# Kernel optimization log

Measured on AMD Instinct MI355X. Metric: run time of the kernel, lower is better.

The kernel has to match this reference:

```python
import jax, jax.numpy as jnp
import numpy as np

N = 1024    # num_points
HID = 1024  # Hamiltonian MLP hidden width


def setup_inputs() -> dict:
    key = jax.random.key(0)
    ks = jax.random.split(key, 6)
    def w(k, shape, fan_in):
        return jax.random.normal(k, shape, dtype=jnp.float32) / np.float32(np.sqrt(fan_in))
    return {
        "x": jax.random.normal(ks[0], (N,), dtype=jnp.float32),
        "q": jax.random.normal(ks[1], (N,), dtype=jnp.float32),
        "p": jax.random.normal(ks[2], (N,), dtype=jnp.float32),
        "W1": w(ks[3], (3 * N, HID), 3 * N),
        "b1": jnp.zeros((HID,), dtype=jnp.float32),
        "W2": w(ks[4], (HID, HID), HID),
        "b2": jnp.zeros((HID,), dtype=jnp.float32),
        "W3": w(ks[5], (HID, 1), HID),
        "b3": jnp.zeros((1,), dtype=jnp.float32),
    }


def _hamiltonian(z, W1, b1, W2, b2, W3, b3):
    # H: R^{3N} -> scalar (matches self.H(cat([x,q,p])).sum())
    h = jnp.tanh(z @ W1 + b1)
    h = jnp.tanh(h @ W2 + b2)
    return jnp.sum(h @ W3 + b3)


def reference(x, q, p, W1, b1, W2, b2, W3, b3):
    n = x.shape[0]

    def grads_qp(x_):
        # (dH/dq, dH/dp) as a function of x, with q,p closed over
        f = lambda q_, p_: _hamiltonian(jnp.concatenate([x_, q_, p_]), W1, b1, W2, b2, W3, b3)
        return jax.grad(f, argnums=(0, 1))(q, p)  # each [n]

    # Diagonal of cross-Hessian blocks via forward-over-reverse, batched over
    # all n basis directions at once (replaces the per-index autograd loop).
    eye = jnp.eye(n, dtype=x.dtype)

    def diag_entry(e_i, i):
        _, (dgq, dgp) = jax.jvp(grads_qp, (x,), (e_i,))
        return dgq[i], dgp[i]  # d2H/(dx_i dq_i), d2H/(dx_i dp_i)

    dH_dq_dx, dH_dp_dx = jax.vmap(diag_entry)(eye, jnp.arange(n))  # each [n]
    return dH_dp_dx, -dH_dq_dx
```

## Files before the change

kernel.cpp:

```cpp
#include <hip/hip_runtime.h>
#include <math.h>

typedef unsigned short u16;
typedef __bf16 bf16x8 __attribute__((ext_vector_type(8)));
typedef float f32x4 __attribute__((ext_vector_type(4)));

__device__ inline u16 bf16_rn(float x) {
    unsigned u = __float_as_uint(x);
    return (u16)((u + 0x7FFFu + ((u >> 16) & 1u)) >> 16);
}
__device__ inline uint2 pack4(u16 a, u16 b, u16 c, u16 d) {
    uint2 r;
    r.x = (unsigned)a | ((unsigned)b << 16);
    r.y = (unsigned)c | ((unsigned)d << 16);
    return r;
}
__device__ inline uint2 pack4f(float a, float b, float c, float d) {
    return pack4(bf16_rn(a), bf16_rn(b), bf16_rn(c), bf16_rn(d));
}
__device__ inline f32x4 mfma16(bf16x8 a, bf16x8 b, f32x4 c) {
    return __builtin_amdgcn_mfma_f32_16x16x32_bf16(a, b, c, 0, 0, 0);
}

__global__ __launch_bounds__(256) void k_pre(const float* __restrict__ x,
                                             const float* __restrict__ q,
                                             const float* __restrict__ p,
                                             const float* __restrict__ W1,
                                             u16* __restrict__ Ah,
                                             float* __restrict__ Upart,
                                             float* __restrict__ out,
                                             float* __restrict__ Vacc) {
    int b = blockIdx.x, t = threadIdx.x;
    if (b < 1024) {
        int idx = (b * 256 + t) * 4;
        float4 v = *(const float4*)(W1 + idx);
        *(uint2*)&Ah[idx] = pack4f(v.x, v.y, v.z, v.w);
    } else if (b < 1216) {
        int jc = b - 1024;
        int k = (jc & 3) * 256 + t;
        int j0 = (jc >> 2) * 64;
        __shared__ float zs[64];
        if (t < 64) {
            int j = j0 + t;
            zs[t] = (j < 1024) ? x[j] : (j < 2048 ? q[j - 1024] : p[j - 2048]);
        }
        __syncthreads();
        float acc = 0.f;
#pragma unroll 8
        for (int j = 0; j < 64; ++j) acc += zs[j] * W1[(j0 + j) * 1024 + k];
        Upart[(jc >> 2) * 1024 + k] = acc;
    } else {
        int idx = ((b - 1216) * 256 + t) * 4;
        if (idx < 2048) *(float4*)(out + idx) = make_float4(0.f, 0.f, 0.f, 0.f);
        else *(float4*)(Vacc + idx - 2048) = make_float4(0.f, 0.f, 0.f, 0.f);
    }
}

__global__ __launch_bounds__(256) void k_w2v(const float* __restrict__ W2,
                                             const float* __restrict__ b1,
                                             const float* __restrict__ Upart,
                                             float* __restrict__ H1g, float* __restrict__ D1g,
                                             u16* __restrict__ W2h,
                                             u16* __restrict__ WTh,
                                             float* __restrict__ Vacc) {
    __shared__ float T[64][65];
    __shared__ float hs[64], ds[64];
    int k0 = blockIdx.y * 64, m0 = blockIdx.x * 64;
    int t = threadIdx.x;
    if (t < 64) {
        float u = 0.f;
#pragma unroll 8
        for (int c = 0; c < 48; ++c) u += Upart[c * 1024 + k0 + t];
        float h = tanhf(u + b1[k0 + t]);
        hs[t] = h;
        ds[t] = 1.f - h * h;
        if (m0 == 0) { H1g[k0 + t] = h; D1g[k0 + t] = 1.f - h * h; }
    }
    __syncthreads();
    int rr = t >> 4, cc = (t & 15) * 4;
    float4 vp = make_float4(0.f, 0.f, 0.f, 0.f);
#pragma unroll
    for (int j = 0; j < 4; ++j) {
        int r = rr + j * 16;
        float4 v = *(const float4*)(W2 + (k0 + r) * 1024 + m0 + cc);
        T[r][cc + 0] = v.x; T[r][cc + 1] = v.y; T[r][cc + 2] = v.z; T[r][cc + 3] = v.w;
        *(uint2*)&W2h[(k0 + r) * 1024 + m0 + cc] = pack4f(v.x, v.y, v.z, v.w);
        float hk = hs[r];
        vp.x += hk * v.x; vp.y += hk * v.y; vp.z += hk * v.z; vp.w += hk * v.w;
    }
    vp.x += __shfl_xor(vp.x, 16); vp.y += __shfl_xor(vp.y, 16);
    vp.z += __shfl_xor(vp.z, 16); vp.w += __shfl_xor(vp.w, 16);
    vp.x += __shfl_xor(vp.x, 32); vp.y += __shfl_xor(vp.y, 32);
    vp.z += __shfl_xor(vp.z, 32); vp.w += __shfl_xor(vp.w, 32);
    if (((t & 63) >> 4) == 0) {
        atomicAdd(&Vacc[m0 + cc + 0], vp.x);
        atomicAdd(&Vacc[m0 + cc + 1], vp.y);
        atomicAdd(&Vacc[m0 + cc + 2], vp.z);
        atomicAdd(&Vacc[m0 + cc + 3], vp.w);
    }
    __syncthreads();
#pragma unroll
    for (int j = 0; j < 4; ++j) {
        int mrow = rr + j * 16;
        float f0 = T[cc + 0][mrow] * ds[cc + 0];
        float f1 = T[cc + 1][mrow] * ds[cc + 1];
        float f2 = T[cc + 2][mrow] * ds[cc + 2];
        float f3 = T[cc + 3][mrow] * ds[cc + 3];
        *(uint2*)&WTh[(m0 + mrow) * 1024 + k0 + cc] = pack4f(f0, f1, f2, f3);
    }
}

#define LDK 68
__global__ __launch_bounds__(512) void k_gemm1(const u16* __restrict__ Ah,
                                               const u16* __restrict__ Bh,
                                               const float* __restrict__ Vacc,
                                               const float* __restrict__ b2,
                                               const float* __restrict__ W3,
                                               const float* __restrict__ W2,
                                               const float* __restrict__ H1,
                                               const float* __restrict__ D1,
                                               float* __restrict__ Avec,
                                               u16* __restrict__ Sh) {
    __shared__ u16 As[2][64 * LDK];
    __shared__ u16 Bs[2][64 * LDK];
    __shared__ float sv[1024];
    int tid = threadIdx.x;
    if (blockIdx.x == 16) {
        int kbase = blockIdx.y * 64;
#pragma unroll
        for (int j = 0; j < 2; ++j) {
            int m = tid + j * 512;
            float h = tanhf(Vacc[m] + b2[m]);
            sv[m] = (1.f - h * h) * W3[m];
        }
        __syncthreads();
        int g = tid >> 3, sub = tid & 7;
        int k = kbase + g;
        const float* wrow = W2 + k * 1024 + sub * 128;
        const float* svp = sv + sub * 128;
        float acc = 0.f;
#pragma unroll 8
        for (int j = 0; j < 128; ++j) acc += wrow[j] * svp[j];
        acc += __shfl_xor(acc, 1);
        acc += __shfl_xor(acc, 2);
        acc += __shfl_xor(acc, 4);
        if (sub == 0) Avec[k] = -2.f * H1[k] * D1[k] * acc;
        return;
    }
    int lane = tid & 63, wv = tid >> 6;
    int kh = wv >> 2, wy = (wv >> 1) & 1, wx = wv & 1;
    int i0 = blockIdx.y * 64, m0 = blockIdx.x * 64;
    int srow = tid >> 3, sseg = (tid & 7) * 8;
    int ldso = srow * LDK + sseg;
    const u16* ap = Ah + (i0 + srow) * 1024 + sseg;
    const u16* bp = Bh + (m0 + srow) * 1024 + sseg;
    int tx = lane & 15, qy = lane >> 4;
    int koff = kh * 32 + qy * 8;
    int raA[2], rbB[2];
    raA[0] = (wy * 32 + tx) * LDK + koff;
    raA[1] = raA[0] + 16 * LDK;
    rbB[0] = (wx * 32 + tx) * LDK + koff;
    rbB[1] = rbB[0] + 16 * LDK;
    f32x4 acc[2][2];
#pragma unroll
    for (int a = 0; a < 2; ++a)
#pragma unroll
        for (int b = 0; b < 2; ++b) acc[a][b] = (f32x4){0.f, 0.f, 0.f, 0.f};

    *(uint4*)&As[0][ldso] = *(const uint4*)(ap);
    *(uint4*)&Bs[0][ldso] = *(const uint4*)(bp);

    for (int k0 = 0; k0 < 1024; k0 += 64) {
        int buf = (k0 >> 6) & 1;
        int kn = (k0 + 64) & 1023;
        uint4 pa = *(const uint4*)(ap + kn);
        uint4 pc = *(const uint4*)(bp + kn);
        __syncthreads();
        bf16x8 aH0 = *(const bf16x8*)&As[buf][raA[0]];
        bf16x8 aH1 = *(const bf16x8*)&As[buf][raA[1]];
        bf16x8 bH0 = *(const bf16x8*)&Bs[buf][rbB[0]];
        bf16x8 bH1 = *(const bf16x8*)&Bs[buf][rbB[1]];
        acc[0][0] = mfma16(aH0, bH0, acc[0][0]);
        acc[0][1] = mfma16(aH0, bH1, acc[0][1]);
        acc[1][0] = mfma16(aH1, bH0, acc[1][0]);
        acc[1][1] = mfma16(aH1, bH1, acc[1][1]);
        int nb = buf ^ 1;
        *(uint4*)&As[nb][ldso] = pa;
        *(uint4*)&Bs[nb][ldso] = pc;
    }
    __syncthreads();
    f32x4* mrg = (f32x4*)&As[0][0];
    if (kh == 1) {
#pragma unroll
        for (int si = 0; si < 2; ++si)
#pragma unroll
            for (int sj = 0; sj < 2; ++sj)
                mrg[(((wy * 2 + wx) * 4 + si * 2 + sj) * 4 + qy) * 16 + tx] = acc[si][sj];
    }
    __syncthreads();
    if (kh == 0) {
#pragma unroll
        for (int si = 0; si < 2; ++si)
#pragma unroll
            for (int sj = 0; sj < 2; ++sj) {
                f32x4 o = mrg[(((wy * 2 + wx) * 4 + si * 2 + sj) * 4 + qy) * 16 + tx];
                acc[si][sj][0] += o[0]; acc[si][sj][1] += o[1];
                acc[si][sj][2] += o[2]; acc[si][sj][3] += o[3];
            }
#pragma unroll
        for (int sj = 0; sj < 2; ++sj) {
            int m = m0 + wx * 32 + sj * 16 + tx;
            float hv = tanhf(Vacc[m] + b2[m]);
            float d2 = 1.f - hv * hv;
            float cm = -2.f * hv * d2 * W3[m];
#pragma unroll
            for (int si = 0; si < 2; ++si) {
                int ib = i0 + wy * 32 + si * 16 + qy * 4;
#pragma unroll
                for (int r = 0; r < 4; ++r)
                    Sh[(ib + r) * 1024 + m] = bf16_rn(acc[si][sj][r] * cm);
            }
        }
    }
}

__global__ __launch_bounds__(512) void k_gemm2(const u16* __restrict__ Sh,
                                               const u16* __restrict__ W2h,
                                               const float* __restrict__ W1,
                                               const float* __restrict__ D1,
                                               const float* __restrict__ Avec,
                                               float* __restrict__ out) {
    __shared__ u16 As[2][64 * LDK];
    __shared__ u16 Bs[2][64 * LDK];
    int tid = threadIdx.x, lane = tid & 63, wv = tid >> 6;
    int kh = wv >> 2, wy = (wv >> 1) & 1, wx = wv & 1;
    int i0 = blockIdx.y * 64, k0g = blockIdx.x * 64;
    int srow = tid >> 3, sseg = (tid & 7) * 8;
    int ldso = srow * LDK + sseg;
    const u16* ap = Sh + (i0 + srow) * 1024 + sseg;
    const u16* bp = W2h + (k0g + srow) * 1024 + sseg;
    int tx = lane & 15, qy = lane >> 4;
    int koff = kh * 32 + qy * 8;
    int raA[2], rbB[2];
    raA[0] = (wy * 32 + tx) * LDK + koff;
    raA[1] = raA[0] + 16 * LDK;
    rbB[0] = (wx * 32 + tx) * LDK + koff;
    rbB[1] = rbB[0] + 16 * LDK;
    f32x4 acc[2][2];
#pragma unroll
    for (int a = 0; a < 2; ++a)
#pragma unroll
        for (int b = 0; b < 2; ++b) acc[a][b] = (f32x4){0.f, 0.f, 0.f, 0.f};

    *(uint4*)&As[0][ldso] = *(const uint4*)(ap);
    *(uint4*)&Bs[0][ldso] = *(const uint4*)(bp);

    for (int m0 = 0; m0 < 1024; m0 += 64) {
        int buf = (m0 >> 6) & 1;
        int mn = (m0 + 64) & 1023;
        uint4 pa = *(const uint4*)(ap + mn);
        uint4 pc = *(const uint4*)(bp + mn);
        __syncthreads();
        bf16x8 aH0 = *(const bf16x8*)&As[buf][raA[0]];
        bf16x8 aH1 = *(const bf16x8*)&As[buf][raA[1]];
        bf16x8 bH0 = *(const bf16x8*)&Bs[buf][rbB[0]];
        bf16x8 bH1 = *(const bf16x8*)&Bs[buf][rbB[1]];
        acc[0][0] = mfma16(aH0, bH0, acc[0][0]);
        acc[0][1] = mfma16(aH0, bH1, acc[0][1]);
        acc[1][0] = mfma16(aH1, bH0, acc[1][0]);
        acc[1][1] = mfma16(aH1, bH1, acc[1][1]);
        int nb = buf ^ 1;
        *(uint4*)&As[nb][ldso] = pa;
        *(uint4*)&Bs[nb][ldso] = pc;
    }
    __syncthreads();
    f32x4* mrg = (f32x4*)&As[0][0];
    if (kh == 1) {
#pragma unroll
        for (int si = 0; si < 2; ++si)
#pragma unroll
            for (int sj = 0; sj < 2; ++sj)
                mrg[(((wy * 2 + wx) * 4 + si * 2 + sj) * 4 + qy) * 16 + tx] = acc[si][sj];
    }
    __syncthreads();
    if (kh == 0) {
#pragma unroll
        for (int si = 0; si < 2; ++si)
#pragma unroll
            for (int sj = 0; sj < 2; ++sj) {
                f32x4 o = mrg[(((wy * 2 + wx) * 4 + si * 2 + sj) * 4 + qy) * 16 + tx];
                acc[si][sj][0] += o[0]; acc[si][sj][1] += o[1];
                acc[si][sj][2] += o[2]; acc[si][sj][3] += o[3];
            }
        int kk[2];
        float d1v[2], avv[2];
#pragma unroll
        for (int sj = 0; sj < 2; ++sj) {
            kk[sj] = k0g + wx * 32 + sj * 16 + tx;
            d1v[sj] = D1[kk[sj]];
            avv[sj] = Avec[kk[sj]];
        }
#pragma unroll
        for (int si = 0; si < 2; ++si) {
            int ib = i0 + wy * 32 + si * 16 + qy * 4;
#pragma unroll
            for (int r = 0; r < 4; ++r) {
                int i = ib + r;
                float pq = 0.f, pp = 0.f;
#pragma unroll
                for (int sj = 0; sj < 2; ++sj) {
                    int k = kk[sj];
                    float dr = avv[sj] * W1[i * 1024 + k] + d1v[sj] * acc[si][sj][r];
                    pq += W1[(1024 + i) * 1024 + k] * dr;
                    pp += W1[(2048 + i) * 1024 + k] * dr;
                }
                for (int o = 1; o < 16; o <<= 1) {
                    pq += __shfl_xor(pq, o);
                    pp += __shfl_xor(pp, o);
                }
                if (tx == 0) {
                    atomicAdd(&out[i], pp);
                    atomicAdd(&out[1024 + i], -pq);
                }
            }
        }
    }
}

extern "C" void kernel_launch(void* const* d_in, const int* in_sizes, int n_in,
                              void* d_out, int out_size, void* d_ws, size_t ws_size,
                              hipStream_t stream) {
    const float* x = (const float*)d_in[0];
    const float* q = (const float*)d_in[1];
    const float* p = (const float*)d_in[2];
    const float* W1 = (const float*)d_in[3];
    const float* b1 = (const float*)d_in[4];
    const float* W2 = (const float*)d_in[5];
    const float* b2 = (const float*)d_in[6];
    const float* W3 = (const float*)d_in[7];
    float* out = (float*)d_out;
    float* ws = (float*)d_ws;
    float* H1 = ws, *D1 = ws + 1024, *Avec = ws + 2048, *Vacc = ws + 3072;
    float* Upart = ws + 4096;
    u16* u0 = (u16*)(ws + 65536);
    u16* Ah = u0;
    u16* WTh = u0 + 1048576;
    u16* W2h = u0 + 2097152;
    u16* Sh = u0 + 3145728;

    k_pre<<<1219, 256, 0, stream>>>(x, q, p, W1, Ah, Upart, out, Vacc);
    k_w2v<<<dim3(16, 16), 256, 0, stream>>>(W2, b1, Upart, H1, D1, W2h, WTh, Vacc);
    k_gemm1<<<dim3(17, 16), 512, 0, stream>>>(Ah, WTh, Vacc, b2, W3, W2, H1, D1, Avec, Sh);
    k_gemm2<<<dim3(16, 16), 512, 0, stream>>>(Sh, W2h, W1, D1, Avec, out);
}
```

Measured before the change: 120.0 us.

## Fuse W1 bf16 conversion into matvec, parallelize Upart reduce, deepen GEMM prefetch

The first 1024 rows of W1 are now converted to bf16 inside the z·W1 partial matvec blocks that already read them, so the separate conversion blocks go away and W1 is read once instead of twice. k_w2v spreads the 48-way Upart reduction over all 256 threads in four groups instead of only 64 threads. Both GEMM kernels prefetch global tiles two iterations ahead instead of one, which uses more registers. The fused conversion loop stores scalar u16 values with less parallelism (192 blocks), which may limit bandwidth.

```diff
diff --git a/kernel.cpp b/kernel.cpp
--- a/kernel.cpp
+++ b/kernel.cpp
@@ -31,12 +31,8 @@
                                              float* __restrict__ out,
                                              float* __restrict__ Vacc) {
     int b = blockIdx.x, t = threadIdx.x;
-    if (b < 1024) {
-        int idx = (b * 256 + t) * 4;
-        float4 v = *(const float4*)(W1 + idx);
-        *(uint2*)&Ah[idx] = pack4f(v.x, v.y, v.z, v.w);
-    } else if (b < 1216) {
-        int jc = b - 1024;
+    if (b < 192) {
+        int jc = b;
         int k = (jc & 3) * 256 + t;
         int j0 = (jc >> 2) * 64;
         __shared__ float zs[64];
@@ -46,11 +42,20 @@
         }
         __syncthreads();
         float acc = 0.f;
+        if (j0 < 1024) {
 #pragma unroll 8
-        for (int j = 0; j < 64; ++j) acc += zs[j] * W1[(j0 + j) * 1024 + k];
+            for (int j = 0; j < 64; ++j) {
+                float v = W1[(j0 + j) * 1024 + k];
+                Ah[(j0 + j) * 1024 + k] = bf16_rn(v);
+                acc += zs[j] * v;
+            }
+        } else {
+#pragma unroll 8
+            for (int j = 0; j < 64; ++j) acc += zs[j] * W1[(j0 + j) * 1024 + k];
+        }
         Upart[(jc >> 2) * 1024 + k] = acc;
     } else {
-        int idx = ((b - 1216) * 256 + t) * 4;
+        int idx = ((b - 192) * 256 + t) * 4;
         if (idx < 2048) *(float4*)(out + idx) = make_float4(0.f, 0.f, 0.f, 0.f);
         else *(float4*)(Vacc + idx - 2048) = make_float4(0.f, 0.f, 0.f, 0.f);
     }
@@ -65,12 +70,19 @@
                                              float* __restrict__ Vacc) {
     __shared__ float T[64][65];
     __shared__ float hs[64], ds[64];
+    __shared__ float red[4][64];
     int k0 = blockIdx.y * 64, m0 = blockIdx.x * 64;
     int t = threadIdx.x;
+    {
+        int lk = t & 63, g = t >> 6;
+        float u = 0.f;
+#pragma unroll
+        for (int c = 0; c < 12; ++c) u += Upart[(g * 12 + c) * 1024 + k0 + lk];
+        red[g][lk] = u;
+    }
+    __syncthreads();
     if (t < 64) {
-        float u = 0.f;
-#pragma unroll 8
-        for (int c = 0; c < 48; ++c) u += Upart[c * 1024 + k0 + t];
+        float u = red[0][t] + red[1][t] + red[2][t] + red[3][t];
         float h = tanhf(u + b1[k0 + t]);
         hs[t] = h;
         ds[t] = 1.f - h * h;
@@ -167,14 +179,16 @@
 #pragma unroll
         for (int b = 0; b < 2; ++b) acc[a][b] = (f32x4){0.f, 0.f, 0.f, 0.f};
 
+    uint4 pa1 = *(const uint4*)(ap + 64);
+    uint4 pc1 = *(const uint4*)(bp + 64);
     *(uint4*)&As[0][ldso] = *(const uint4*)(ap);
     *(uint4*)&Bs[0][ldso] = *(const uint4*)(bp);
 
     for (int k0 = 0; k0 < 1024; k0 += 64) {
         int buf = (k0 >> 6) & 1;
-        int kn = (k0 + 64) & 1023;
-        uint4 pa = *(const uint4*)(ap + kn);
-        uint4 pc = *(const uint4*)(bp + kn);
+        int kn2 = (k0 + 128) & 1023;
+        uint4 pa2 = *(const uint4*)(ap + kn2);
+        uint4 pc2 = *(const uint4*)(bp + kn2);
         __syncthreads();
         bf16x8 aH0 = *(const bf16x8*)&As[buf][raA[0]];
         bf16x8 aH1 = *(const bf16x8*)&As[buf][raA[1]];
@@ -185,8 +199,9 @@
         acc[1][0] = mfma16(aH1, bH0, acc[1][0]);
         acc[1][1] = mfma16(aH1, bH1, acc[1][1]);
         int nb = buf ^ 1;
-        *(uint4*)&As[nb][ldso] = pa;
-        *(uint4*)&Bs[nb][ldso] = pc;
+        *(uint4*)&As[nb][ldso] = pa1;
+        *(uint4*)&Bs[nb][ldso] = pc1;
+        pa1 = pa2; pc1 = pc2;
     }
     __syncthreads();
     f32x4* mrg = (f32x4*)&As[0][0];
@@ -252,14 +267,16 @@
 #pragma unroll
         for (int b = 0; b < 2; ++b) acc[a][b] = (f32x4){0.f, 0.f, 0.f, 0.f};
 
+    uint4 pa1 = *(const uint4*)(ap + 64);
+    uint4 pc1 = *(const uint4*)(bp + 64);
     *(uint4*)&As[0][ldso] = *(const uint4*)(ap);
     *(uint4*)&Bs[0][ldso] = *(const uint4*)(bp);
 
     for (int m0 = 0; m0 < 1024; m0 += 64) {
         int buf = (m0 >> 6) & 1;
-        int mn = (m0 + 64) & 1023;
-        uint4 pa = *(const uint4*)(ap + mn);
-        uint4 pc = *(const uint4*)(bp + mn);
+        int mn2 = (m0 + 128) & 1023;
+        uint4 pa2 = *(const uint4*)(ap + mn2);
+        uint4 pc2 = *(const uint4*)(bp + mn2);
         __syncthreads();
         bf16x8 aH0 = *(const bf16x8*)&As[buf][raA[0]];
         bf16x8 aH1 = *(const bf16x8*)&As[buf][raA[1]];
@@ -270,8 +287,9 @@
         acc[1][0] = mfma16(aH1, bH0, acc[1][0]);
         acc[1][1] = mfma16(aH1, bH1, acc[1][1]);
         int nb = buf ^ 1;
-        *(uint4*)&As[nb][ldso] = pa;
-        *(uint4*)&Bs[nb][ldso] = pc;
+        *(uint4*)&As[nb][ldso] = pa1;
+        *(uint4*)&Bs[nb][ldso] = pc1;
+        pa1 = pa2; pc1 = pc2;
     }
     __syncthreads();
     f32x4* mrg = (f32x4*)&As[0][0];
@@ -348,7 +366,7 @@
     u16* W2h = u0 + 2097152;
     u16* Sh = u0 + 3145728;
 
-    k_pre<<<1219, 256, 0, stream>>>(x, q, p, W1, Ah, Upart, out, Vacc);
+    k_pre<<<195, 256, 0, stream>>>(x, q, p, W1, Ah, Upart, out, Vacc);
     k_w2v<<<dim3(16, 16), 256, 0, stream>>>(W2, b1, Upart, H1, D1, W2h, WTh, Vacc);
     k_gemm1<<<dim3(17, 16), 512, 0, stream>>>(Ah, WTh, Vacc, b2, W3, W2, H1, D1, Avec, Sh);
     k_gemm2<<<dim3(16, 16), 512, 0, stream>>>(Sh, W2h, W1, D1, Avec, out);
```

After: 119.2 us. No clear change (-0.7%).
